# Kernel tuning notes

Hardware: AMD Instinct MI355X
Metric: run time of the kernel (lower is better)

The kernel has to match this reference:

```python
import jax, jax.numpy as jnp
import numpy as np

# Dimensions
B, S, F, PATCH, D, H, NL, DFF, HOR = 512, 336, 12, 6, 512, 8, 6, 2048, 24
NP = S // PATCH        # 56 temporal patches
DH = D // H            # head dim = 64
EPS = 1e-5


def layer_norm(x, g, b):
    m = jnp.mean(x, axis=-1, keepdims=True)
    v = jnp.mean(jnp.square(x - m), axis=-1, keepdims=True)
    return (x - m) * jax.lax.rsqrt(v + EPS) * g + b


def alibi_bias(n_heads, n):
    # slopes = 2^(-8h/H), h = 1..H (standard ALiBi, H power of 2)
    slopes = 2.0 ** (-8.0 * jnp.arange(1, n_heads + 1, dtype=jnp.float32) / n_heads)
    pos = jnp.arange(n, dtype=jnp.float32)
    dist = jnp.abs(pos[:, None] - pos[None, :])         # [n, n]
    return -slopes[:, None, None] * dist                # [H, n, n]


def setup_inputs() -> dict:
    key = jax.random.key(0)
    ks = jax.random.split(key, 16)
    g = lambda k, shape: jax.random.normal(k, shape, dtype=jnp.float32) * 0.02
    return {
        "x": jax.random.normal(ks[0], (B, S, F), dtype=jnp.float32),
        "patch_W": g(ks[1], (PATCH * F, D)),
        "patch_b": jnp.zeros((D,), jnp.float32),
        "pos": g(ks[2], (NP, D)),
        "ln1_g": jnp.ones((NL, D), jnp.float32),
        "ln1_b": jnp.zeros((NL, D), jnp.float32),
        "Wq": g(ks[3], (NL, D, D)), "bq": jnp.zeros((NL, D), jnp.float32),
        "Wk": g(ks[4], (NL, D, D)), "bk": jnp.zeros((NL, D), jnp.float32),
        "Wv": g(ks[5], (NL, D, D)), "bv": jnp.zeros((NL, D), jnp.float32),
        "Wo": g(ks[6], (NL, D, D)), "bo": jnp.zeros((NL, D), jnp.float32),
        "ln2_g": jnp.ones((NL, D), jnp.float32),
        "ln2_b": jnp.zeros((NL, D), jnp.float32),
        "W1": g(ks[7], (NL, D, DFF)), "b1": jnp.zeros((NL, DFF), jnp.float32),
        "W2": g(ks[8], (NL, DFF, D)), "b2": jnp.zeros((NL, D), jnp.float32),
        "fn_g": jnp.ones((D,), jnp.float32),
        "fn_b": jnp.zeros((D,), jnp.float32),
        "head_W": g(ks[9], (D, HOR)),
        "head_b": jnp.zeros((HOR,), jnp.float32),
    }


def reference(x, patch_W, patch_b, pos, ln1_g, ln1_b, Wq, bq, Wk, bk, Wv, bv,
              Wo, bo, ln2_g, ln2_b, W1, b1, W2, b2, fn_g, fn_b, head_W, head_b):
    # Temporal patch embedding: (B,S,F) -> (B,NP,PATCH*F) -> Linear -> +pos
    h = x.reshape(B, NP, PATCH * F) @ patch_W + patch_b + pos  # [B, NP, D]
    bias = alibi_bias(H, NP)                                   # [H, NP, NP]
    scale = 1.0 / np.sqrt(DH).astype(np.float32)
    for l in range(NL):
        # Pre-LN multi-head attention with ALiBi temporal decay bias
        hn = layer_norm(h, ln1_g[l], ln1_b[l])
        q = (hn @ Wq[l] + bq[l]).reshape(B, NP, H, DH)
        k = (hn @ Wk[l] + bk[l]).reshape(B, NP, H, DH)
        v = (hn @ Wv[l] + bv[l]).reshape(B, NP, H, DH)
        sc = jnp.einsum('bqhd,bkhd->bhqk', q, k) * scale + bias[None]
        a = jax.nn.softmax(sc, axis=-1)
        o = jnp.einsum('bhqk,bkhd->bqhd', a, v).reshape(B, NP, D)
        h = h + (o @ Wo[l] + bo[l])
        # Pre-LN feedforward
        hn2 = layer_norm(h, ln2_g[l], ln2_b[l])
        h = h + (jax.nn.gelu(hn2 @ W1[l] + b1[l]) @ W2[l] + b2[l])
    pooled = jnp.mean(h, axis=1)                               # [B, D]
    out = layer_norm(pooled, fn_g, fn_b) @ head_W + head_b     # [B, HOR]
    return out
```

## Files before the change

### kernel.cpp

```cpp
#include <hip/hip_runtime.h>
#include <hip/hip_bf16.h>
#include <math.h>

#define D_      512
#define NPATCH  56
#define DFF_    2048
#define NLAYER  6
#define HEADS   8
#define DH_     64
#define HOR_    24
#define BATCH_  512
#define NTOK_   (BATCH_ * NPATCH)
#define KPAD    96

typedef __hip_bfloat16 bf16;
typedef __bf16 bf16x8 __attribute__((ext_vector_type(8)));
typedef float  f32x4  __attribute__((ext_vector_type(4)));

__device__ __forceinline__ void gload_lds16(const void* g, void* lds) {
    __builtin_amdgcn_global_load_lds(
        (const __attribute__((address_space(1))) unsigned int*)g,
        (__attribute__((address_space(3))) unsigned int*)lds, 16, 0, 0);
}

__device__ __forceinline__ float block_sum256(float v) {
    __shared__ float sm[4];
    const int lane = threadIdx.x & 63;
    const int w    = threadIdx.x >> 6;
    #pragma unroll
    for (int o = 32; o > 0; o >>= 1) v += __shfl_down(v, o);
    __syncthreads();
    if (lane == 0) sm[w] = v;
    __syncthreads();
    return sm[0] + sm[1] + sm[2] + sm[3];
}

__device__ __forceinline__ float gelu_fast(float xg) {
    const float e = __expf(1.5957691216057308f * (xg + 0.044715f * xg * xg * xg));
    return xg - xg * __builtin_amdgcn_rcpf(1.f + e);
}

__global__ __launch_bounds__(256) void transpose_bf16_k(
    const float* __restrict__ in, bf16* __restrict__ out, int R, int C,
    size_t in_ls, size_t out_ls)
{
    __shared__ float t[32][33];
    in  += (size_t)blockIdx.z * in_ls;
    out += (size_t)blockIdx.z * out_ls;
    const int c0 = blockIdx.x * 32, r0 = blockIdx.y * 32;
    const int x = threadIdx.x & 31, y = threadIdx.x >> 5;
    #pragma unroll
    for (int i = 0; i < 4; i++)
        t[y + i * 8][x] = in[(size_t)(r0 + y + i * 8) * C + c0 + x];
    __syncthreads();
    #pragma unroll
    for (int i = 0; i < 4; i++)
        out[(size_t)(c0 + y + i * 8) * R + r0 + x] = __float2bfloat16(t[x][y + i * 8]);
}

__global__ __launch_bounds__(256) void pwt_k(
    const float* __restrict__ W, bf16* __restrict__ out)
{
    const int idx = blockIdx.x * 256 + threadIdx.x;
    if (idx >= D_ * KPAD) return;
    const int n = idx / KPAD, kk = idx % KPAD;
    out[idx] = (kk < 72) ? __float2bfloat16(W[kk * D_ + n]) : __float2bfloat16(0.f);
}

__global__ __launch_bounds__(256) void xpad_k(
    const float* __restrict__ x, bf16* __restrict__ out)
{
    const size_t idx = (size_t)blockIdx.x * 256 + threadIdx.x;
    if (idx >= (size_t)NTOK_ * KPAD) return;
    const size_t row = idx / KPAD;
    const int kk = (int)(idx - row * KPAD);
    out[idx] = (kk < 72) ? __float2bfloat16(x[row * 72 + kk]) : __float2bfloat16(0.f);
}

__global__ __launch_bounds__(256) void bqkv_k(
    const float* __restrict__ bq, const float* __restrict__ bk,
    const float* __restrict__ bv, float* __restrict__ o)
{
    const int idx = blockIdx.x * 256 + threadIdx.x;
    if (idx >= NLAYER * 3 * D_) return;
    const int l = idx / (3 * D_), n = idx % (3 * D_);
    float v;
    if      (n < D_)     v = bq[l * D_ + n];
    else if (n < 2 * D_) v = bk[l * D_ + n - D_];
    else                 v = bv[l * D_ + n - 2 * D_];
    o[idx] = v;
}

__global__ __launch_bounds__(256) void layernorm_bf16_k(
    const float* __restrict__ x, const float* __restrict__ g,
    const float* __restrict__ b, bf16* __restrict__ y)
{
    const int w = threadIdx.x >> 6, lane = threadIdx.x & 63;
    const size_t row = (size_t)blockIdx.x * 4 + w;
    const float* xr = x + row * D_ + lane * 8;
    const float4 a0 = *(const float4*)xr;
    const float4 a1 = *(const float4*)(xr + 4);
    float s = a0.x + a0.y + a0.z + a0.w + a1.x + a1.y + a1.z + a1.w;
    #pragma unroll
    for (int o = 32; o > 0; o >>= 1) s += __shfl_xor(s, o);
    const float mean = s * (1.f / 512.f);
    float d[8] = {a0.x - mean, a0.y - mean, a0.z - mean, a0.w - mean,
                  a1.x - mean, a1.y - mean, a1.z - mean, a1.w - mean};
    float v = 0.f;
    #pragma unroll
    for (int i = 0; i < 8; i++) v += d[i] * d[i];
    #pragma unroll
    for (int o = 32; o > 0; o >>= 1) v += __shfl_xor(v, o);
    const float rstd = rsqrtf(v * (1.f / 512.f) + 1e-5f);
    const float4 g0 = *(const float4*)(g + lane * 8);
    const float4 g1 = *(const float4*)(g + lane * 8 + 4);
    const float4 b0 = *(const float4*)(b + lane * 8);
    const float4 b1 = *(const float4*)(b + lane * 8 + 4);
    const float gg[8] = {g0.x, g0.y, g0.z, g0.w, g1.x, g1.y, g1.z, g1.w};
    const float bb[8] = {b0.x, b0.y, b0.z, b0.w, b1.x, b1.y, b1.z, b1.w};
    bf16x8 o8;
    #pragma unroll
    for (int i = 0; i < 8; i++) o8[i] = (__bf16)(d[i] * rstd * gg[i] + bb[i]);
    *(bf16x8*)((__bf16*)y + row * D_ + lane * 8) = o8;
}

template<bool OUT_BF16, bool GELU, bool RESID, bool POS, bool QKVSPLIT>
__global__ __launch_bounds__(256, 3) void gemm_bf16_k(
    const bf16* __restrict__ A, const bf16* __restrict__ Bt,
    const float* __restrict__ bias, const float* __restrict__ resid,
    const float* __restrict__ pos, void* __restrict__ Cp,
    bf16* __restrict__ vt, int M, int N, int K, int nx)
{
    __shared__ __align__(16) bf16 As[3][128 * 32];
    __shared__ __align__(16) bf16 Bs[3][128 * 32];
    const int tid  = threadIdx.x;
    const int wid  = tid >> 6;
    const int lane = tid & 63;

    const int nwg = gridDim.x;
    const int q8 = nwg >> 3, r8 = nwg & 7;
    const int xcd = blockIdx.x & 7, idx8 = blockIdx.x >> 3;
    const int swz = (xcd < r8 ? xcd * (q8 + 1) : r8 * (q8 + 1) + (xcd - r8) * q8) + idx8;
    const int n0 = (swz % nx) * 128;
    const int m0 = (swz / nx) * 128;
    const int wr = wid >> 1, wc = wid & 1;

    f32x4 acc[4][4];
    #pragma unroll
    for (int m = 0; m < 4; m++)
        #pragma unroll
        for (int n = 0; n < 4; n++) acc[m][n] = f32x4{0.f, 0.f, 0.f, 0.f};

    const int srow = lane >> 2;
    const int schunk = ((lane & 3) ^ ((lane >> 3) & 3)) * 8;
    const bf16* gA = A  + (size_t)(m0 + wid * 32 + srow) * K + schunk;
    const bf16* gB = Bt + (size_t)(n0 + wid * 32 + srow) * K + schunk;
    const size_t k16 = (size_t)16 * K;
    const int s0 = (wid * 2 + 0) * 512, s1 = (wid * 2 + 1) * 512;

    const int fr = lane & 15;
    const int qg = lane >> 4;
    const int roff = fr * 32 + ((qg ^ ((fr >> 1) & 3)) * 8);

    const int nt = K >> 5;
    {
        gload_lds16(gA,            &As[0][s0]);
        gload_lds16(gA + k16,      &As[0][s1]);
        gload_lds16(gB,            &Bs[0][s0]);
        gload_lds16(gB + k16,      &Bs[0][s1]);
        gload_lds16(gA + 32,       &As[1][s0]);
        gload_lds16(gA + 32 + k16, &As[1][s1]);
        gload_lds16(gB + 32,       &Bs[1][s0]);
        gload_lds16(gB + 32 + k16, &Bs[1][s1]);
    }

    int cur = 0, nxt = 2;
    for (int t = 0; t < nt; t++) {
        if (t < nt - 1) asm volatile("s_waitcnt vmcnt(4)" ::: "memory");
        else            asm volatile("s_waitcnt vmcnt(0)" ::: "memory");
        __builtin_amdgcn_s_barrier();
        __builtin_amdgcn_sched_barrier(0);
        bf16x8 af[4], bg[4];
        #pragma unroll
        for (int m = 0; m < 4; m++) af[m] = *(const bf16x8*)&As[cur][(wr * 4 + m) * 512 + roff];
        #pragma unroll
        for (int n = 0; n < 4; n++) bg[n] = *(const bf16x8*)&Bs[cur][(wc * 4 + n) * 512 + roff];
        if (t + 2 < nt) {
            const int kn = (t + 2) << 5;
            gload_lds16(gA + kn,       &As[nxt][s0]);
            gload_lds16(gA + kn + k16, &As[nxt][s1]);
            gload_lds16(gB + kn,       &Bs[nxt][s0]);
            gload_lds16(gB + kn + k16, &Bs[nxt][s1]);
        }
        #pragma unroll
        for (int m = 0; m < 4; m++)
            #pragma unroll
            for (int n = 0; n < 4; n++)
                acc[m][n] = __builtin_amdgcn_mfma_f32_16x16x32_bf16(af[m], bg[n], acc[m][n], 0, 0, 0);
        cur = (cur == 2) ? 0 : cur + 1;
        nxt = (nxt == 2) ? 0 : nxt + 1;
    }

    const int rq = qg * 4;
    #pragma unroll
    for (int m = 0; m < 4; m++) {
        #pragma unroll
        for (int n = 0; n < 4; n++) {
            const int col = n0 + wc * 64 + n * 16 + fr;
            const float bcol = bias[col];
            #pragma unroll
            for (int j = 0; j < 4; j++) {
                const int row = m0 + wr * 64 + m * 16 + rq + j;
                float c = acc[m][n][j] + bcol;
                if (GELU)  c = gelu_fast(c);
                if (RESID) c += resid[(size_t)row * N + col];
                if (POS)   c += pos[(size_t)(row % NPATCH) * D_ + col];
                if (QKVSPLIT) {
                    if (col < 1024) {
                        ((bf16*)Cp)[(size_t)row * 1024 + col] = __float2bfloat16(c);
                    } else {
                        const int c2 = col - 1024, hh = c2 >> 6, dd = c2 & 63;
                        const int bb = row / NPATCH, pp = row - bb * NPATCH;
                        vt[(((size_t)bb * 8 + hh) * 64 + dd) * 64 + pp] = __float2bfloat16(c);
                    }
                } else if (OUT_BF16) {
                    ((bf16*)Cp)[(size_t)row * N + col] = __float2bfloat16(c);
                } else {
                    ((float*)Cp)[(size_t)row * N + col] = c;
                }
            }
        }
    }
}

__global__ __launch_bounds__(256) void attn_mfma_k(
    const bf16* __restrict__ qk, const bf16* __restrict__ vt,
    bf16* __restrict__ ao)
{
    __shared__ __align__(16) bf16 St[4][64 * 72];
    const int tid  = threadIdx.x;
    const int w    = tid >> 6, lane = tid & 63;
    const int bh   = blockIdx.x * 4 + w;
    const int b    = bh >> 3, hh = bh & 7;
    const int fr   = lane & 15;
    const int qg   = lane >> 4;
    const int kc   = qg * 8;

    const bf16* Qb = qk + (size_t)b * NPATCH * 1024 + hh * 64;
    const bf16* Kb = Qb + 512;
    const bf16* Vb = vt + (size_t)bh * 4096;

    bf16x8 qf[4][2], kf[4][2];
    #pragma unroll
    for (int m = 0; m < 4; m++)
        #pragma unroll
        for (int ks = 0; ks < 2; ks++) {
            qf[m][ks] = *(const bf16x8*)&Qb[(size_t)(m * 16 + fr) * 1024 + ks * 32 + kc];
            kf[m][ks] = *(const bf16x8*)&Kb[(size_t)(m * 16 + fr) * 1024 + ks * 32 + kc];
        }

    f32x4 acc[4][4];
    #pragma unroll
    for (int m = 0; m < 4; m++)
        #pragma unroll
        for (int n = 0; n < 4; n++) acc[m][n] = f32x4{0.f, 0.f, 0.f, 0.f};
    #pragma unroll
    for (int ks = 0; ks < 2; ks++)
        #pragma unroll
        for (int m = 0; m < 4; m++)
            #pragma unroll
            for (int n = 0; n < 4; n++)
                acc[m][n] = __builtin_amdgcn_mfma_f32_16x16x32_bf16(qf[m][ks], kf[n][ks], acc[m][n], 0, 0, 0);

    bf16x8 vf[4][2];
    #pragma unroll
    for (int n = 0; n < 4; n++)
        #pragma unroll
        for (int ks = 0; ks < 2; ks++)
            vf[n][ks] = *(const bf16x8*)&Vb[(size_t)(n * 16 + fr) * 64 + ks * 32 + kc];

    const float slope = exp2f(-(float)(hh + 1));
    bf16* Sw = St[w];
    #pragma unroll
    for (int m = 0; m < 4; m++) {
        #pragma unroll
        for (int j = 0; j < 4; j++) {
            const int r = m * 16 + qg * 4 + j;
            float s[4];
            #pragma unroll
            for (int n = 0; n < 4; n++) {
                const int col = n * 16 + fr;
                float sv = acc[m][n][j] * 0.125f - slope * fabsf((float)(r - col));
                s[n] = (col >= NPATCH) ? -1e30f : sv;
            }
            float mx = fmaxf(fmaxf(s[0], s[1]), fmaxf(s[2], s[3]));
            mx = fmaxf(mx, __shfl_xor(mx, 1));
            mx = fmaxf(mx, __shfl_xor(mx, 2));
            mx = fmaxf(mx, __shfl_xor(mx, 4));
            mx = fmaxf(mx, __shfl_xor(mx, 8));
            float p[4], sum = 0.f;
            #pragma unroll
            for (int n = 0; n < 4; n++) { p[n] = __expf(s[n] - mx); sum += p[n]; }
            sum += __shfl_xor(sum, 1);
            sum += __shfl_xor(sum, 2);
            sum += __shfl_xor(sum, 4);
            sum += __shfl_xor(sum, 8);
            const float inv = 1.f / sum;
            #pragma unroll
            for (int n = 0; n < 4; n++)
                Sw[r * 72 + n * 16 + fr] = __float2bfloat16(p[n] * inv);
        }
    }

    #pragma unroll
    for (int m = 0; m < 4; m++)
        #pragma unroll
        for (int n = 0; n < 4; n++) acc[m][n] = f32x4{0.f, 0.f, 0.f, 0.f};
    #pragma unroll
    for (int m = 0; m < 4; m++)
        #pragma unroll
        for (int ks = 0; ks < 2; ks++) {
            const bf16x8 pf = *(const bf16x8*)&Sw[(m * 16 + fr) * 72 + ks * 32 + kc];
            #pragma unroll
            for (int n = 0; n < 4; n++)
                acc[m][n] = __builtin_amdgcn_mfma_f32_16x16x32_bf16(pf, vf[n][ks], acc[m][n], 0, 0, 0);
        }

    bf16* Ob = ao + (size_t)b * NPATCH * 512 + hh * 64;
    #pragma unroll
    for (int m = 0; m < 4; m++)
        #pragma unroll
        for (int j = 0; j < 4; j++) {
            const int r = m * 16 + qg * 4 + j;
            if (r < NPATCH)
                #pragma unroll
                for (int n = 0; n < 4; n++)
                    Ob[(size_t)r * 512 + n * 16 + fr] = __float2bfloat16(acc[m][n][j]);
        }
}

__global__ __launch_bounds__(256) void meanpool_k(
    const float* __restrict__ h, float* __restrict__ pooled)
{
    const int b = blockIdx.x;
    for (int d = threadIdx.x; d < D_; d += 256) {
        float acc = 0.f;
        #pragma unroll
        for (int p = 0; p < NPATCH; p++)
            acc += h[(size_t)b * NPATCH * D_ + (size_t)p * D_ + d];
        pooled[(size_t)b * D_ + d] = acc * (1.f / (float)NPATCH);
    }
}

__global__ __launch_bounds__(256) void head_k(
    const float* __restrict__ pooled, const float* __restrict__ g,
    const float* __restrict__ bb, const float* __restrict__ hW,
    const float* __restrict__ hb, float* __restrict__ out)
{
    const int b = blockIdx.x;
    __shared__ float row[D_];
    const int tid = threadIdx.x;
    const float v0 = pooled[(size_t)b * D_ + tid];
    const float v1 = pooled[(size_t)b * D_ + tid + 256];
    const float mean = block_sum256(v0 + v1) * (1.f / 512.f);
    const float d0 = v0 - mean, d1 = v1 - mean;
    const float var = block_sum256(d0 * d0 + d1 * d1) * (1.f / 512.f);
    const float rstd = rsqrtf(var + 1e-5f);
    row[tid]       = d0 * rstd * g[tid]       + bb[tid];
    row[tid + 256] = d1 * rstd * g[tid + 256] + bb[tid + 256];
    __syncthreads();
    if (tid < HOR_) {
        float acc = hb[tid];
        for (int kk = 0; kk < D_; kk++) acc = fmaf(row[kk], hW[kk * HOR_ + tid], acc);
        out[(size_t)b * HOR_ + tid] = acc;
    }
}

extern "C" void kernel_launch(void* const* d_in, const int* in_sizes, int n_in,
                              void* d_out, int out_size, void* d_ws, size_t ws_size,
                              hipStream_t stream)
{
    const float* x       = (const float*)d_in[0];
    const float* patch_W = (const float*)d_in[1];
    const float* patch_b = (const float*)d_in[2];
    const float* pos     = (const float*)d_in[3];
    const float* ln1_g   = (const float*)d_in[4];
    const float* ln1_b   = (const float*)d_in[5];
    const float* Wq      = (const float*)d_in[6];
    const float* bq      = (const float*)d_in[7];
    const float* Wk      = (const float*)d_in[8];
    const float* bk      = (const float*)d_in[9];
    const float* Wv      = (const float*)d_in[10];
    const float* bv      = (const float*)d_in[11];
    const float* Wo      = (const float*)d_in[12];
    const float* bo      = (const float*)d_in[13];
    const float* ln2_g   = (const float*)d_in[14];
    const float* ln2_b   = (const float*)d_in[15];
    const float* W1      = (const float*)d_in[16];
    const float* b1      = (const float*)d_in[17];
    const float* W2      = (const float*)d_in[18];
    const float* b2      = (const float*)d_in[19];
    const float* fn_g    = (const float*)d_in[20];
    const float* fn_b    = (const float*)d_in[21];
    const float* head_W  = (const float*)d_in[22];
    const float* head_b  = (const float*)d_in[23];
    float* out = (float*)d_out;

    const size_t WELEM  = (size_t)D_ * D_;
    const size_t WFELEM = (size_t)D_ * DFF_;
    bf16* wqkvt = (bf16*)d_ws;
    bf16* wot   = wqkvt + (size_t)NLAYER * 3 * WELEM;
    bf16* w1t   = wot   + (size_t)NLAYER * WELEM;
    bf16* w2t   = w1t   + (size_t)NLAYER * WFELEM;
    bf16* pwt   = w2t   + (size_t)NLAYER * WFELEM;
    float* bqkv = (float*)(pwt + (size_t)D_ * KPAD);
    bf16* xpad  = (bf16*)(bqkv + NLAYER * 3 * D_);
    char* wend  = (char*)(xpad + (size_t)NTOK_ * KPAD);
    const size_t FIXED = (size_t)(wend - (char*)d_ws);

    int BC = 16;
    for (int cand = BATCH_; cand >= 16; cand >>= 1) {
        const size_t need = FIXED + (size_t)cand * (56 * 6144 + 65536 + 2048);
        if (need <= ws_size) { BC = cand; break; }
    }
    const int nChunks = BATCH_ / BC;
    const int CT = BC * NPATCH;
    const size_t TD = (size_t)CT * D_;

    float* h    = (float*)wend;
    bf16*  hn   = (bf16*)(h + TD);
    bf16*  qk   = hn + TD;
    bf16*  ao   = qk + (size_t)CT * 1024;
    bf16*  vt   = ao + TD;
    bf16*  mid  = qk;
    float* pooled = (float*)(vt + (size_t)BC * 8 * 64 * 64);

    transpose_bf16_k<<<dim3(16, 16, NLAYER), 256, 0, stream>>>(
        Wq, wqkvt,                 D_, D_, WELEM, 3 * WELEM);
    transpose_bf16_k<<<dim3(16, 16, NLAYER), 256, 0, stream>>>(
        Wk, wqkvt + WELEM,         D_, D_, WELEM, 3 * WELEM);
    transpose_bf16_k<<<dim3(16, 16, NLAYER), 256, 0, stream>>>(
        Wv, wqkvt + 2 * WELEM,     D_, D_, WELEM, 3 * WELEM);
    transpose_bf16_k<<<dim3(16, 16, NLAYER), 256, 0, stream>>>(
        Wo, wot,                   D_, D_, WELEM, WELEM);
    transpose_bf16_k<<<dim3(64, 16, NLAYER), 256, 0, stream>>>(
        W1, w1t,                   D_, DFF_, WFELEM, WFELEM);
    transpose_bf16_k<<<dim3(16, 64, NLAYER), 256, 0, stream>>>(
        W2, w2t,                   DFF_, D_, WFELEM, WFELEM);
    pwt_k<<<(D_ * KPAD + 255) / 256, 256, 0, stream>>>(patch_W, pwt);
    bqkv_k<<<(NLAYER * 3 * D_ + 255) / 256, 256, 0, stream>>>(bq, bk, bv, bqkv);
    xpad_k<<<((size_t)NTOK_ * KPAD + 255) / 256, 256, 0, stream>>>(x, xpad);

    const int g1n = (D_ / 128) * (CT / 128);
    const int gqn = (3 * D_ / 128) * (CT / 128);
    const int g2n = (DFF_ / 128) * (CT / 128);

    for (int c = 0; c < nChunks; c++) {
        const size_t tok0 = (size_t)c * CT;

        gemm_bf16_k<false, false, false, true, false><<<g1n, 256, 0, stream>>>(
            xpad + tok0 * KPAD, pwt, patch_b, nullptr, pos, h, nullptr,
            CT, D_, KPAD, D_ / 128);

        for (int l = 0; l < NLAYER; l++) {
            layernorm_bf16_k<<<CT / 4, 256, 0, stream>>>(h, ln1_g + l * D_, ln1_b + l * D_, hn);
            gemm_bf16_k<true, false, false, false, true><<<gqn, 256, 0, stream>>>(
                hn, wqkvt + (size_t)l * 3 * WELEM, bqkv + l * 3 * D_, nullptr, nullptr,
                qk, vt, CT, 3 * D_, D_, 3 * D_ / 128);
            attn_mfma_k<<<BC * 2, 256, 0, stream>>>(qk, vt, ao);
            gemm_bf16_k<false, false, true, false, false><<<g1n, 256, 0, stream>>>(
                ao, wot + (size_t)l * WELEM, bo + l * D_, h, nullptr, h, nullptr,
                CT, D_, D_, D_ / 128);
            layernorm_bf16_k<<<CT / 4, 256, 0, stream>>>(h, ln2_g + l * D_, ln2_b + l * D_, hn);
            gemm_bf16_k<true, true, false, false, false><<<g2n, 256, 0, stream>>>(
                hn, w1t + (size_t)l * WFELEM, b1 + l * DFF_, nullptr, nullptr,
                mid, nullptr, CT, DFF_, D_, DFF_ / 128);
            gemm_bf16_k<false, false, true, false, false><<<g1n, 256, 0, stream>>>(
                mid, w2t + (size_t)l * WFELEM, b2 + l * D_, h, nullptr, h, nullptr,
                CT, D_, DFF_, D_ / 128);
        }

        meanpool_k<<<BC, 256, 0, stream>>>(h, pooled);
        head_k<<<BC, 256, 0, stream>>>(pooled, fn_g, fn_b, head_W, head_b,
                                       out + (size_t)c * BC * HOR_);
    }
}
```

Before: 2.229 ms.

## Load GEMM B fragments directly to registers and fuse meanpool into head kernel

The GEMM no longer stages the weight (B) tile through LDS. Each wave loads its B fragments straight from global memory into registers and prefetches the next k-step while the current MFMAs run. Halving LDS use allows launch bounds of four blocks per CU, and s_setprio is raised around the MFMA block. The meanpool kernel is folded into the head kernel, which removes one launch and the pooled buffer. The cost is that B reads are no longer shared across the two wave rows through LDS, so global/L2 traffic and per-thread register pressure go up.

```diff
diff --git a/kernel.cpp b/kernel.cpp
--- a/kernel.cpp
+++ b/kernel.cpp
@@ -125,14 +125,13 @@
 }
 
 template<bool OUT_BF16, bool GELU, bool RESID, bool POS, bool QKVSPLIT>
-__global__ __launch_bounds__(256, 3) void gemm_bf16_k(
+__global__ __launch_bounds__(256, 4) void gemm_bf16_k(
     const bf16* __restrict__ A, const bf16* __restrict__ Bt,
     const float* __restrict__ bias, const float* __restrict__ resid,
     const float* __restrict__ pos, void* __restrict__ Cp,
     bf16* __restrict__ vt, int M, int N, int K, int nx)
 {
     __shared__ __align__(16) bf16 As[3][128 * 32];
-    __shared__ __align__(16) bf16 Bs[3][128 * 32];
     const int tid  = threadIdx.x;
     const int wid  = tid >> 6;
     const int lane = tid & 63;
@@ -153,53 +152,58 @@
 
     const int srow = lane >> 2;
     const int schunk = ((lane & 3) ^ ((lane >> 3) & 3)) * 8;
-    const bf16* gA = A  + (size_t)(m0 + wid * 32 + srow) * K + schunk;
-    const bf16* gB = Bt + (size_t)(n0 + wid * 32 + srow) * K + schunk;
+    const bf16* gA = A + (size_t)(m0 + wid * 32 + srow) * K + schunk;
     const size_t k16 = (size_t)16 * K;
     const int s0 = (wid * 2 + 0) * 512, s1 = (wid * 2 + 1) * 512;
 
     const int fr = lane & 15;
     const int qg = lane >> 4;
     const int roff = fr * 32 + ((qg ^ ((fr >> 1) & 3)) * 8);
+    const bf16* gBf = Bt + (size_t)(n0 + wc * 64 + fr) * K + qg * 8;
+    const size_t n16K = (size_t)16 * K;
 
     const int nt = K >> 5;
-    {
-        gload_lds16(gA,            &As[0][s0]);
-        gload_lds16(gA + k16,      &As[0][s1]);
-        gload_lds16(gB,            &Bs[0][s0]);
-        gload_lds16(gB + k16,      &Bs[0][s1]);
-        gload_lds16(gA + 32,       &As[1][s0]);
-        gload_lds16(gA + 32 + k16, &As[1][s1]);
-        gload_lds16(gB + 32,       &Bs[1][s0]);
-        gload_lds16(gB + 32 + k16, &Bs[1][s1]);
-    }
+
+    #define STAGE_A(buf, kt)  do { const bf16* _s = gA + ((kt) << 5); \
+        gload_lds16(_s,       &As[buf][s0]);                          \
+        gload_lds16(_s + k16, &As[buf][s1]); } while (0)
+
+    STAGE_A(0, 0);
+    STAGE_A(1, 1);
+    bf16x8 bg[4], bgn[4];
+    #pragma unroll
+    for (int n = 0; n < 4; n++) bg[n] = *(const bf16x8*)(gBf + n * n16K);
 
     int cur = 0, nxt = 2;
+    #pragma unroll 2
     for (int t = 0; t < nt; t++) {
-        if (t < nt - 1) asm volatile("s_waitcnt vmcnt(4)" ::: "memory");
-        else            asm volatile("s_waitcnt vmcnt(0)" ::: "memory");
+        asm volatile("s_waitcnt vmcnt(6)" ::: "memory");
         __builtin_amdgcn_s_barrier();
         __builtin_amdgcn_sched_barrier(0);
-        bf16x8 af[4], bg[4];
+        bf16x8 af[4];
         #pragma unroll
         for (int m = 0; m < 4; m++) af[m] = *(const bf16x8*)&As[cur][(wr * 4 + m) * 512 + roff];
-        #pragma unroll
-        for (int n = 0; n < 4; n++) bg[n] = *(const bf16x8*)&Bs[cur][(wc * 4 + n) * 512 + roff];
-        if (t + 2 < nt) {
-            const int kn = (t + 2) << 5;
-            gload_lds16(gA + kn,       &As[nxt][s0]);
-            gload_lds16(gA + kn + k16, &As[nxt][s1]);
-            gload_lds16(gB + kn,       &Bs[nxt][s0]);
-            gload_lds16(gB + kn + k16, &Bs[nxt][s1]);
-        }
+        if (t + 2 < nt) STAGE_A(nxt, t + 2);
+        if (t + 1 < nt) {
+            const bf16* bsrc = gBf + ((t + 1) << 5);
+            #pragma unroll
+            for (int n = 0; n < 4; n++) bgn[n] = *(const bf16x8*)(bsrc + n * n16K);
+        }
+        asm volatile("s_waitcnt lgkmcnt(0)" ::: "memory");
+        __builtin_amdgcn_sched_barrier(0);
+        __builtin_amdgcn_s_setprio(1);
         #pragma unroll
         for (int m = 0; m < 4; m++)
             #pragma unroll
             for (int n = 0; n < 4; n++)
                 acc[m][n] = __builtin_amdgcn_mfma_f32_16x16x32_bf16(af[m], bg[n], acc[m][n], 0, 0, 0);
+        __builtin_amdgcn_s_setprio(0);
+        #pragma unroll
+        for (int n = 0; n < 4; n++) bg[n] = bgn[n];
         cur = (cur == 2) ? 0 : cur + 1;
         nxt = (nxt == 2) ? 0 : nxt + 1;
     }
+    #undef STAGE_A
 
     const int rq = qg * 4;
     #pragma unroll
@@ -339,29 +343,23 @@
         }
 }
 
-__global__ __launch_bounds__(256) void meanpool_k(
-    const float* __restrict__ h, float* __restrict__ pooled)
-{
-    const int b = blockIdx.x;
-    for (int d = threadIdx.x; d < D_; d += 256) {
-        float acc = 0.f;
-        #pragma unroll
-        for (int p = 0; p < NPATCH; p++)
-            acc += h[(size_t)b * NPATCH * D_ + (size_t)p * D_ + d];
-        pooled[(size_t)b * D_ + d] = acc * (1.f / (float)NPATCH);
-    }
-}
-
 __global__ __launch_bounds__(256) void head_k(
-    const float* __restrict__ pooled, const float* __restrict__ g,
+    const float* __restrict__ h, const float* __restrict__ g,
     const float* __restrict__ bb, const float* __restrict__ hW,
     const float* __restrict__ hb, float* __restrict__ out)
 {
     const int b = blockIdx.x;
     __shared__ float row[D_];
     const int tid = threadIdx.x;
-    const float v0 = pooled[(size_t)b * D_ + tid];
-    const float v1 = pooled[(size_t)b * D_ + tid + 256];
+    float v0 = 0.f, v1 = 0.f;
+    #pragma unroll
+    for (int p = 0; p < NPATCH; p++) {
+        const float* hr = h + (size_t)b * NPATCH * D_ + (size_t)p * D_;
+        v0 += hr[tid];
+        v1 += hr[tid + 256];
+    }
+    v0 *= (1.f / (float)NPATCH);
+    v1 *= (1.f / (float)NPATCH);
     const float mean = block_sum256(v0 + v1) * (1.f / 512.f);
     const float d0 = v0 - mean, d1 = v1 - mean;
     const float var = block_sum256(d0 * d0 + d1 * d1) * (1.f / 512.f);
@@ -420,7 +418,7 @@
 
     int BC = 16;
     for (int cand = BATCH_; cand >= 16; cand >>= 1) {
-        const size_t need = FIXED + (size_t)cand * (56 * 6144 + 65536 + 2048);
+        const size_t need = FIXED + (size_t)cand * (56 * 6144 + 65536);
         if (need <= ws_size) { BC = cand; break; }
     }
     const int nChunks = BATCH_ / BC;
@@ -433,7 +431,6 @@
     bf16*  ao   = qk + (size_t)CT * 1024;
     bf16*  vt   = ao + TD;
     bf16*  mid  = qk;
-    float* pooled = (float*)(vt + (size_t)BC * 8 * 64 * 64);
 
     transpose_bf16_k<<<dim3(16, 16, NLAYER), 256, 0, stream>>>(
         Wq, wqkvt,                 D_, D_, WELEM, 3 * WELEM);
@@ -480,8 +477,7 @@
                 CT, D_, DFF_, D_ / 128);
         }
 
-        meanpool_k<<<BC, 256, 0, stream>>>(h, pooled);
-        head_k<<<BC, 256, 0, stream>>>(pooled, fn_g, fn_b, head_W, head_b,
+        head_k<<<BC, 256, 0, stream>>>(h, fn_g, fn_b, head_W, head_b,
                                        out + (size_t)c * BC * HOR_);
     }
 }
```

After: 3.439 ms. 54.3% more time.
